# Optimization experiments

Hardware: AMD Instinct MI355X
Metric: run time of the kernel (lower is better)

## Reference

```python
import jax, jax.numpy as jnp
import numpy as np

B, T, E = 2, 4096, 1024
H = 16
D = E // H  # head_len = 64


def setup_inputs() -> dict:
    key = jax.random.key(0)
    ks = jax.random.split(key, 6)
    s = 1.0 / np.sqrt(E)
    return {
        "x": jax.random.normal(ks[0], (B, T, E), dtype=jnp.float32),
        # torch nn.Linear weights: shape (out, in), y = x @ W.T
        "Wq": jax.random.uniform(ks[1], (E, E), jnp.float32, -s, s),
        "Wk": jax.random.uniform(ks[2], (E, E), jnp.float32, -s, s),
        "Wv": jax.random.uniform(ks[3], (E, E), jnp.float32, -s, s),
        "Wo": jax.random.uniform(ks[4], (E, E), jnp.float32, -s, s),
        "bo": jax.random.uniform(ks[5], (E,), jnp.float32, -s, s),
    }


def reference(x, Wq, Wk, Wv, Wo, bo):
    Bx, Tx, Ex = x.shape
    q = x @ Wq.T
    k = x @ Wk.T
    v = x @ Wv.T
    # (B, T, H, D) -> (B, H, T, D)
    q = q.reshape(Bx, Tx, H, D).transpose(0, 2, 1, 3)
    k = k.reshape(Bx, Tx, H, D).transpose(0, 2, 1, 3)
    v = v.reshape(Bx, Tx, H, D).transpose(0, 2, 1, 3)
    # scores: (B, H, T, T), scaled by sqrt(head_len)
    sim = jnp.einsum("bhqd,bhkd->bhqk", q, k) / jnp.sqrt(jnp.float32(D))
    causal = jnp.tril(jnp.ones((Tx, Tx), dtype=bool))  # True = keep
    sim = jnp.where(causal[None, None], sim, -jnp.inf)
    attn = jax.nn.softmax(sim, axis=-1)
    # dropout_rate = 0.0 (eval) -> identity
    out = jnp.einsum("bhqk,bhkd->bhqd", attn, v)
    out = out.transpose(0, 2, 1, 3).reshape(Bx, Tx, Ex)
    return out @ Wo.T + bo
```

## Files before the change

kernel.cpp:

```cpp
#include <hip/hip_runtime.h>

typedef unsigned short bf16_t;
typedef __bf16 bf16x8 __attribute__((ext_vector_type(8)));
typedef float  v4f   __attribute__((ext_vector_type(4)));
typedef float  v16f  __attribute__((ext_vector_type(16)));
typedef unsigned u32x2 __attribute__((ext_vector_type(2)));

__device__ __forceinline__ bf16_t f2bf(float f) {
    union { float f; unsigned u; } a; a.f = f;
    unsigned r = a.u + 0x7FFFu + ((a.u >> 16) & 1u);
    return (bf16_t)(r >> 16);
}

__device__ __forceinline__ unsigned cvtpk(float lo, float hi) {
    unsigned r;
    asm("v_cvt_pk_bf16_f32 %0, %1, %2" : "=v"(r) : "v"(lo), "v"(hi));
    return r;
}

__device__ __forceinline__ v16f zero16() {
    v16f z;
#pragma unroll
    for (int i = 0; i < 16; ++i) z[i] = 0.f;
    return z;
}

#define GL16(g, l) __builtin_amdgcn_global_load_lds( \
    (__attribute__((address_space(1))) void*)(g),    \
    (__attribute__((address_space(3))) void*)(l), 16, 0, 0)

#define QSCALE 0.18033688011f

__global__ __launch_bounds__(256) void cvt_all(
    const float4* __restrict__ x,  const float4* __restrict__ wq,
    const float4* __restrict__ wk, const float4* __restrict__ wv,
    const float4* __restrict__ wo,
    ushort4* __restrict__ xb, ushort4* __restrict__ wqkv, ushort4* __restrict__ wob) {
    int i = blockIdx.x * 256 + threadIdx.x;
    const float4* s; ushort4* d; int off;
    if (i < 2097152) { s = x; d = xb; off = i; }
    else {
        int wdx = (i - 2097152) >> 18;
        off = (i - 2097152) & 262143;
        if      (wdx == 0) { s = wq; d = wqkv; }
        else if (wdx == 1) { s = wk; d = wqkv + 262144; }
        else if (wdx == 2) { s = wv; d = wqkv + 524288; }
        else               { s = wo; d = wob; }
    }
    float4 v = s[off];
    ushort4 o;
    o.x = f2bf(v.x); o.y = f2bf(v.y); o.z = f2bf(v.z); o.w = f2bf(v.w);
    d[off] = o;
}

#define GEMM_MAINLOOP(A_, W_)                                                          \
    __shared__ bf16_t SMEM[8192];                                                      \
    bf16_t* As = SMEM; bf16_t* Bs = SMEM + 4096;                                       \
    const int tid = threadIdx.x;                                                       \
    const int w = tid >> 6, lane = tid & 63;                                           \
    const int lrow = lane & 15, lq = lane >> 4;                                        \
    const int nwg_ = gridDim.x * gridDim.y;                                            \
    const int id_ = blockIdx.y * gridDim.x + blockIdx.x;                               \
    const int sid_ = (id_ & 7) * (nwg_ >> 3) + (id_ >> 3);                             \
    const int bxs = sid_ % gridDim.x, bys = sid_ / gridDim.x;                          \
    const int m0 = bys * 128, n0 = bxs * 128;                                          \
    const int srow = w * 16 + (lane >> 2);                                             \
    const int sk = (lane & 3) * 8;                                                     \
    const int wm = (w & 1) * 64, wn = (w >> 1) * 64;                                   \
    v4f acc[4][4];                                                                     \
    _Pragma("unroll") for (int i = 0; i < 4; ++i)                                      \
        _Pragma("unroll") for (int j = 0; j < 4; ++j)                                  \
            acc[i][j] = (v4f){0.f, 0.f, 0.f, 0.f};                                     \
    for (int k0 = 0; k0 < 1024; k0 += 32) {                                            \
        __syncthreads();                                                               \
        GL16(A_ + (size_t)(m0 + srow) * 1024 + k0 + sk,      (char*)As + w * 1024);    \
        GL16(A_ + (size_t)(m0 + 64 + srow) * 1024 + k0 + sk, (char*)As + 4096 + w * 1024); \
        GL16(W_ + (size_t)(n0 + srow) * 1024 + k0 + sk,      (char*)Bs + w * 1024);    \
        GL16(W_ + (size_t)(n0 + 64 + srow) * 1024 + k0 + sk, (char*)Bs + 4096 + w * 1024); \
        __syncthreads();                                                               \
        bf16x8 af[4], bf[4];                                                           \
        _Pragma("unroll") for (int i = 0; i < 4; ++i)                                  \
            af[i] = *(const bf16x8*)&As[(wm + i * 16 + lrow) * 32 + lq * 8];           \
        _Pragma("unroll") for (int j = 0; j < 4; ++j)                                  \
            bf[j] = *(const bf16x8*)&Bs[(wn + j * 16 + lrow) * 32 + lq * 8];           \
        _Pragma("unroll") for (int i = 0; i < 4; ++i)                                  \
            _Pragma("unroll") for (int j = 0; j < 4; ++j)                              \
                acc[i][j] = __builtin_amdgcn_mfma_f32_16x16x32_bf16(af[i], bf[j],      \
                                                                    acc[i][j], 0, 0, 0); \
    }

__global__ __launch_bounds__(256) void gemm_qkv_kernel(
    const bf16_t* __restrict__ A, const bf16_t* __restrict__ W,
    bf16_t* __restrict__ Qb, bf16_t* __restrict__ Kb, bf16_t* __restrict__ Vtb) {
    GEMM_MAINLOOP(A, W)
    const int x = bxs;
    const int b = m0 >> 12, t0 = m0 & 4095;
    if (x < 8) {
#pragma unroll
        for (int i = 0; i < 4; ++i)
#pragma unroll
            for (int j = 0; j < 4; ++j)
#pragma unroll
                for (int r = 0; r < 4; ++r) {
                    int t = t0 + wm + i * 16 + lq * 4 + r;
                    int n = n0 + wn + j * 16 + lrow;
                    int h = n >> 6, d = n & 63;
                    Qb[(((size_t)b * 16 + h) * 4096 + t) * 64 + d] =
                        f2bf(acc[i][j][r] * QSCALE);
                }
    } else if (x < 16) {
#pragma unroll
        for (int i = 0; i < 4; ++i)
#pragma unroll
            for (int j = 0; j < 4; ++j)
#pragma unroll
                for (int r = 0; r < 4; ++r) {
                    int t = t0 + wm + i * 16 + lq * 4 + r;
                    int nn = n0 + wn + j * 16 + lrow - 1024;
                    int h = nn >> 6, d = nn & 63;
                    Kb[(((size_t)b * 16 + h) * 4096 + t) * 64 + d] = f2bf(acc[i][j][r]);
                }
    } else {
        const int d0 = n0 - 2048;
#pragma unroll 1
        for (int p = 0; p < 2; ++p) {
            __syncthreads();
            if ((w >> 1) == p) {
#pragma unroll
                for (int i = 0; i < 4; ++i)
#pragma unroll
                    for (int j = 0; j < 4; ++j) {
                        int row = j * 16 + lrow;
                        int swz = (row & 7) << 1;
                        int g = (wm >> 2) + i * 4 + lq;
                        uint2 u;
                        u.x = (unsigned)f2bf(acc[i][j][0]) | ((unsigned)f2bf(acc[i][j][1]) << 16);
                        u.y = (unsigned)f2bf(acc[i][j][2]) | ((unsigned)f2bf(acc[i][j][3]) << 16);
                        *(uint2*)&SMEM[row * 128 + ((g ^ swz) << 2)] = u;
                    }
            }
            __syncthreads();
#pragma unroll
            for (int uu = 0; uu < 4; ++uu) {
                int unit = tid + 256 * uu;
                int row = unit >> 4, seg = unit & 15;
                uint4 val = *(const uint4*)&SMEM[row * 128 + ((seg ^ (row & 7)) << 3)];
                *(uint4*)&Vtb[((size_t)b * 1024 + d0 + p * 64 + row) * 4096 + t0 + seg * 8] = val;
            }
        }
    }
}

__global__ __launch_bounds__(256) void gemm_out_kernel(
    const bf16_t* __restrict__ A, const bf16_t* __restrict__ W,
    const float* __restrict__ bo, float* __restrict__ out) {
    GEMM_MAINLOOP(A, W)
#pragma unroll
    for (int j = 0; j < 4; ++j) {
        int n = n0 + wn + j * 16 + lrow;
        float bias = bo[n];
#pragma unroll
        for (int i = 0; i < 4; ++i)
#pragma unroll
            for (int r = 0; r < 4; ++r) {
                int m = m0 + wm + i * 16 + lq * 4 + r;
                out[(size_t)m * 1024 + n] = acc[i][j][r] + bias;
            }
    }
}

__global__ __launch_bounds__(256, 2) void attn_kernel(
    const bf16_t* __restrict__ Q, const bf16_t* __restrict__ K,
    const bf16_t* __restrict__ Vt, bf16_t* __restrict__ O) {
    __shared__ bf16_t Kls[2][64 * 64];
    __shared__ bf16_t Vls[2][64 * 64];
    const int tid = threadIdx.x;
    const int w = tid >> 6, lane = tid & 63;
    const int l31 = lane & 31, lh = lane >> 5;
    const int bh = blockIdx.y;
    const int g = blockIdx.x;

    const bf16_t* Qh = Q + (size_t)bh * (4096 * 64);
    const bf16_t* Kh = K + (size_t)bh * (4096 * 64);
    const bf16_t* Vh = Vt + (size_t)bh * (64 * 4096);
    const int b = bh >> 4, h = bh & 15;

    const int svrow = lane >> 3;
    const int sg8 = ((lane & 7) ^ svrow) * 8;
    const int rx = l31 & 7;

    bf16x8 ones;
#pragma unroll
    for (int i = 0; i < 8; ++i) ones[i] = (__bf16)1.0f;

#pragma unroll 1
    for (int mem = 0; mem < 2; ++mem) {
        const int j = mem ? (31 - g) : g;
        const int q0 = j * 128;
        const int q0w = q0 + w * 32;
        const int nt = 2 * j + 2;
        const int wlast = 2 * j + (w >> 1);
        const int qglob = q0w + l31;

        bf16x8 qf[4];
#pragma unroll
        for (int dk = 0; dk < 4; ++dk)
            qf[dk] = *(const bf16x8*)&Qh[(size_t)(q0w + l31) * 64 + dk * 16 + lh * 8];

        v16f oacc0 = zero16(), oacc1 = zero16(), lacc = zero16();

        auto stage = [&](int kt, int buf) {
            const int kc0 = kt << 6;
#pragma unroll
            for (int i = 0; i < 2; ++i) {
                int r0 = w * 16 + i * 8;
                GL16(Kh + (size_t)(kc0 + r0 + svrow) * 64 + sg8, (char*)&Kls[buf][r0 * 64]);
                GL16(Vh + (size_t)(r0 + svrow) * 4096 + kc0 + sg8, (char*)&Vls[buf][r0 * 64]);
            }
        };

        stage(0, 0);
        for (int kt = 0; kt < nt; ++kt) {
            const int buf = kt & 1;
            __syncthreads();
            if (kt + 1 < nt) stage(kt + 1, buf ^ 1);
            if (kt > wlast) continue;
            const int kc0 = kt << 6;
            const bool diag = (kt == wlast);

            bf16x8 kf[2][4];
#pragma unroll
            for (int th = 0; th < 2; ++th)
#pragma unroll
                for (int dk = 0; dk < 4; ++dk)
                    kf[th][dk] = *(const bf16x8*)
                        &Kls[buf][(th * 32 + l31) * 64 + (((dk * 2 + lh) ^ rx) * 8)];
            bf16x8 vf[2][4];
#pragma unroll
            for (int db = 0; db < 2; ++db)
#pragma unroll
                for (int kb = 0; kb < 4; ++kb)
                    vf[db][kb] = *(const bf16x8*)
                        &Vls[buf][(db * 32 + l31) * 64 + (((kb * 2 + lh) ^ rx) * 8)];

            v16f st0 = zero16(), st1 = zero16();
            __builtin_amdgcn_s_setprio(1);
#pragma unroll
            for (int dk = 0; dk < 4; ++dk) {
                st0 = __builtin_amdgcn_mfma_f32_32x32x16_bf16(kf[0][dk], qf[dk], st0, 0, 0, 0);
                st1 = __builtin_amdgcn_mfma_f32_32x32x16_bf16(kf[1][dk], qf[dk], st1, 0, 0, 0);
            }
            __builtin_amdgcn_s_setprio(0);

            bf16x8 pa[4];
#pragma unroll
            for (int th = 0; th < 2; ++th) {
                float p[16];
#pragma unroll
                for (int rr = 0; rr < 16; ++rr) {
                    float pv = __builtin_amdgcn_exp2f(th ? st1[rr] : st0[rr]);
                    if (diag) {
                        int tg = kc0 + th * 32 + (rr & 3) + 8 * (rr >> 2) + 4 * lh;
                        pv = (tg > qglob) ? 0.f : pv;
                    }
                    p[rr] = pv;
                }
#pragma unroll
                for (int kb2 = 0; kb2 < 2; ++kb2) {
                    unsigned x0 = cvtpk(p[kb2 * 8 + 0], p[kb2 * 8 + 1]);
                    unsigned x1 = cvtpk(p[kb2 * 8 + 2], p[kb2 * 8 + 3]);
                    unsigned y0 = cvtpk(p[kb2 * 8 + 4], p[kb2 * 8 + 5]);
                    unsigned y1 = cvtpk(p[kb2 * 8 + 6], p[kb2 * 8 + 7]);
                    u32x2 ra = __builtin_amdgcn_permlane32_swap(x0, y0, false, false);
                    u32x2 rb = __builtin_amdgcn_permlane32_swap(x1, y1, false, false);
                    union { unsigned u[4]; bf16x8 v; } pu;
                    pu.u[0] = ra.x; pu.u[1] = rb.x;
                    pu.u[2] = ra.y; pu.u[3] = rb.y;
                    pa[th * 2 + kb2] = pu.v;
                }
            }

            __builtin_amdgcn_s_setprio(1);
#pragma unroll
            for (int kb = 0; kb < 4; ++kb) {
                lacc  = __builtin_amdgcn_mfma_f32_32x32x16_bf16(pa[kb], ones,       lacc,  0, 0, 0);
                oacc0 = __builtin_amdgcn_mfma_f32_32x32x16_bf16(pa[kb], vf[0][kb], oacc0, 0, 0, 0);
                oacc1 = __builtin_amdgcn_mfma_f32_32x32x16_bf16(pa[kb], vf[1][kb], oacc1, 0, 0, 0);
            }
            __builtin_amdgcn_s_setprio(0);
        }

#pragma unroll
        for (int rr = 0; rr < 16; ++rr) {
            float rl = 1.0f / lacc[rr];
            int q = q0w + (rr & 3) + 8 * (rr >> 2) + 4 * lh;
            size_t o0 = ((size_t)b * 4096 + q) * 1024 + h * 64;
            O[o0 + l31]      = f2bf(oacc0[rr] * rl);
            O[o0 + 32 + l31] = f2bf(oacc1[rr] * rl);
        }
    }
}

extern "C" void kernel_launch(void* const* d_in, const int* in_sizes, int n_in,
                              void* d_out, int out_size, void* d_ws, size_t ws_size,
                              hipStream_t stream) {
    const float* x  = (const float*)d_in[0];
    const float* Wq = (const float*)d_in[1];
    const float* Wk = (const float*)d_in[2];
    const float* Wv = (const float*)d_in[3];
    const float* Wo = (const float*)d_in[4];
    const float* bo = (const float*)d_in[5];
    float* out = (float*)d_out;

    char* ws = (char*)d_ws;
    bf16_t* xb   = (bf16_t*)(ws + 0);
    bf16_t* Wqkv = (bf16_t*)(ws + 16777216);
    bf16_t* Wob  = (bf16_t*)(ws + 23068672);
    bf16_t* Qb   = (bf16_t*)(ws + 25165824);
    bf16_t* Kb   = (bf16_t*)(ws + 41943040);
    bf16_t* Vtb  = (bf16_t*)(ws + 58720256);
    bf16_t* Ob   = (bf16_t*)(ws + 75497472);

    cvt_all<<<12288, 256, 0, stream>>>((const float4*)x, (const float4*)Wq,
                                       (const float4*)Wk, (const float4*)Wv,
                                       (const float4*)Wo,
                                       (ushort4*)xb, (ushort4*)Wqkv, (ushort4*)Wob);

    gemm_qkv_kernel<<<dim3(24, 64), 256, 0, stream>>>(xb, Wqkv, Qb, Kb, Vtb);

    attn_kernel<<<dim3(16, 32), 256, 0, stream>>>(Qb, Kb, Vtb, Ob);

    gemm_out_kernel<<<dim3(8, 64), 256, 0, stream>>>(Ob, Wob, bo, out);
}
```

Before: 311.0 us.

## Double GEMM K-tile with XOR-swizzled LDS, remap attention blocks, drop setprio

The GEMM main loop now stages a K-depth of 64 per iteration instead of 32, using XOR-swizzled LDS rows to avoid bank conflicts. This halves the number of barrier-separated iterations at the cost of twice the shared memory. The attention kernel remaps block IDs so that groups of 8 consecutive blocks cover different heads at the same query tile, which is meant to improve load balance and cache locality. The s_setprio hints around the MFMA sections are also removed.

```diff
diff --git a/kernel.cpp b/kernel.cpp
--- a/kernel.cpp
+++ b/kernel.cpp
@@ -54,8 +54,8 @@
 }
 
 #define GEMM_MAINLOOP(A_, W_)                                                          \
-    __shared__ bf16_t SMEM[8192];                                                      \
-    bf16_t* As = SMEM; bf16_t* Bs = SMEM + 4096;                                       \
+    __shared__ bf16_t SMEM[16384];                                                     \
+    bf16_t* As = SMEM; bf16_t* Bs = SMEM + 8192;                                       \
     const int tid = threadIdx.x;                                                       \
     const int w = tid >> 6, lane = tid & 63;                                           \
     const int lrow = lane & 15, lq = lane >> 4;                                        \
@@ -64,29 +64,35 @@
     const int sid_ = (id_ & 7) * (nwg_ >> 3) + (id_ >> 3);                             \
     const int bxs = sid_ % gridDim.x, bys = sid_ / gridDim.x;                          \
     const int m0 = bys * 128, n0 = bxs * 128;                                          \
-    const int srow = w * 16 + (lane >> 2);                                             \
-    const int sk = (lane & 3) * 8;                                                     \
+    const int svrow = lane >> 3;                      \
+    const int sg8 = ((lane & 7) ^ svrow) * 8;             \
+    const int rx = lrow & 7;                                      \
     const int wm = (w & 1) * 64, wn = (w >> 1) * 64;                                   \
     v4f acc[4][4];                                                                     \
     _Pragma("unroll") for (int i = 0; i < 4; ++i)                                      \
         _Pragma("unroll") for (int j = 0; j < 4; ++j)                                  \
             acc[i][j] = (v4f){0.f, 0.f, 0.f, 0.f};                                     \
-    for (int k0 = 0; k0 < 1024; k0 += 32) {                                            \
+    for (int k0 = 0; k0 < 1024; k0 += 64) {                                            \
         __syncthreads();                                                               \
-        GL16(A_ + (size_t)(m0 + srow) * 1024 + k0 + sk,      (char*)As + w * 1024);    \
-        GL16(A_ + (size_t)(m0 + 64 + srow) * 1024 + k0 + sk, (char*)As + 4096 + w * 1024); \
-        GL16(W_ + (size_t)(n0 + srow) * 1024 + k0 + sk,      (char*)Bs + w * 1024);    \
-        GL16(W_ + (size_t)(n0 + 64 + srow) * 1024 + k0 + sk, (char*)Bs + 4096 + w * 1024); \
+        _Pragma("unroll") for (int ii = 0; ii < 4; ++ii) {                             \
+            int r0 = w * 32 + ii * 8;                                                  \
+            GL16(A_ + (size_t)(m0 + r0 + svrow) * 1024 + k0 + sg8, (char*)As + r0 * 128); \
+            GL16(W_ + (size_t)(n0 + r0 + svrow) * 1024 + k0 + sg8, (char*)Bs + r0 * 128); \
+        }                                                                              \
         __syncthreads();                                                               \
-        bf16x8 af[4], bf[4];                                                           \
+        bf16x8 af[4][2], bf[4][2];                                                     \
         _Pragma("unroll") for (int i = 0; i < 4; ++i)                                  \
-            af[i] = *(const bf16x8*)&As[(wm + i * 16 + lrow) * 32 + lq * 8];           \
-        _Pragma("unroll") for (int j = 0; j < 4; ++j)                                  \
-            bf[j] = *(const bf16x8*)&Bs[(wn + j * 16 + lrow) * 32 + lq * 8];           \
-        _Pragma("unroll") for (int i = 0; i < 4; ++i)                                  \
-            _Pragma("unroll") for (int j = 0; j < 4; ++j)                              \
-                acc[i][j] = __builtin_amdgcn_mfma_f32_16x16x32_bf16(af[i], bf[j],      \
-                                                                    acc[i][j], 0, 0, 0); \
+            _Pragma("unroll") for (int kk = 0; kk < 2; ++kk) {                         \
+                af[i][kk] = *(const bf16x8*)                                           \
+                    &As[(wm + i * 16 + lrow) * 64 + (((kk * 4 + lq) ^ rx) * 8)];       \
+                bf[i][kk] = *(const bf16x8*)                                           \
+                    &Bs[(wn + i * 16 + lrow) * 64 + (((kk * 4 + lq) ^ rx) * 8)];       \
+            }                                                                          \
+        _Pragma("unroll") for (int kk = 0; kk < 2; ++kk)                               \
+            _Pragma("unroll") for (int i = 0; i < 4; ++i)                              \
+                _Pragma("unroll") for (int j = 0; j < 4; ++j)                          \
+                    acc[i][j] = __builtin_amdgcn_mfma_f32_16x16x32_bf16(               \
+                        af[i][kk], bf[j][kk], acc[i][j], 0, 0, 0);                     \
     }
 
 __global__ __launch_bounds__(256) void gemm_qkv_kernel(
@@ -177,8 +183,10 @@
     const int tid = threadIdx.x;
     const int w = tid >> 6, lane = tid & 63;
     const int l31 = lane & 31, lh = lane >> 5;
-    const int bh = blockIdx.y;
-    const int g = blockIdx.x;
+
+    const int id = blockIdx.y * 16 + blockIdx.x;
+    const int g = (id >> 3) & 15;
+    const int bh = (id & 7) + ((id >> 7) << 3);
 
     const bf16_t* Qh = Q + (size_t)bh * (4096 * 64);
     const bf16_t* Kh = K + (size_t)bh * (4096 * 64);
@@ -244,13 +252,11 @@
                         &Vls[buf][(db * 32 + l31) * 64 + (((kb * 2 + lh) ^ rx) * 8)];
 
             v16f st0 = zero16(), st1 = zero16();
-            __builtin_amdgcn_s_setprio(1);
 #pragma unroll
             for (int dk = 0; dk < 4; ++dk) {
                 st0 = __builtin_amdgcn_mfma_f32_32x32x16_bf16(kf[0][dk], qf[dk], st0, 0, 0, 0);
                 st1 = __builtin_amdgcn_mfma_f32_32x32x16_bf16(kf[1][dk], qf[dk], st1, 0, 0, 0);
             }
-            __builtin_amdgcn_s_setprio(0);
 
             bf16x8 pa[4];
 #pragma unroll
@@ -280,14 +286,12 @@
                 }
             }
 
-            __builtin_amdgcn_s_setprio(1);
 #pragma unroll
             for (int kb = 0; kb < 4; ++kb) {
                 lacc  = __builtin_amdgcn_mfma_f32_32x32x16_bf16(pa[kb], ones,       lacc,  0, 0, 0);
                 oacc0 = __builtin_amdgcn_mfma_f32_32x32x16_bf16(pa[kb], vf[0][kb], oacc0, 0, 0, 0);
                 oacc1 = __builtin_amdgcn_mfma_f32_32x32x16_bf16(pa[kb], vf[1][kb], oacc1, 0, 0, 0);
             }
-            __builtin_amdgcn_s_setprio(0);
         }
 
 #pragma unroll
```

Result: slower. 342.8 us (+10.2%).
